# Kernel optimization log

Hardware: AMD Instinct MI355X
Metric: run time of the kernel (lower is better)

Reference implementation:

```python
import jax, jax.numpy as jnp
import numpy as np

RESO = 64
PAD = 0.1
SCALE = 8.0
PLANES = {'xz': (0, 2), 'xy': (0, 1), 'yz': (1, 2)}
PLANE_ORDER = ['xz', 'xy', 'yz']


def normalize_coordinate(p, plane):
    i, j = PLANES[plane]
    xy = jnp.stack([p[..., i], p[..., j]], axis=-1)
    xy = xy / (1.0 + PAD + 1e-3) + 0.5
    return jnp.clip(xy, 0.0, 1.0 - 1e-5)


def coordinate2index(xy, reso):
    x = (xy * reso).astype(jnp.int32)
    return x[..., 0] + reso * x[..., 1]  # (B, T)


def resblock(x, W0, b0, W1, b1, Ws):
    # ResnetBlockFC: fc_1(relu(fc_0(relu(x)))) + shortcut(x)
    net = jnp.maximum(x, 0.0) @ W0 + b0
    dx = jnp.maximum(net, 0.0) @ W1 + b1
    return x @ Ws + dx


def scatter_max_pool(c, idx_flat, num_seg):
    # c: (B, T, h); idx_flat: (B*T,) batch-offset plane indices
    B, T, h = c.shape
    pooled = jax.ops.segment_max(c.reshape(B * T, h), idx_flat, num_segments=num_seg)
    return pooled[idx_flat].reshape(B, T, h)


def plane_feature(p, c, plane):
    # scatter_mean of c into (B, c_dim, RESO, RESO); empty cells -> 0
    B, T, cd = c.shape
    R2 = RESO * RESO
    idx = coordinate2index(normalize_coordinate(p / SCALE, plane), RESO)
    idxf = (idx + jnp.arange(B, dtype=jnp.int32)[:, None] * R2).reshape(-1)
    sums = jax.ops.segment_sum(c.reshape(B * T, cd), idxf, num_segments=B * R2)
    cnt = jax.ops.segment_sum(jnp.ones((B * T,), c.dtype), idxf, num_segments=B * R2)
    mean = sums / jnp.maximum(cnt, 1.0)[:, None]
    return mean.reshape(B, R2, cd).transpose(0, 2, 1).reshape(B, cd, RESO, RESO)


def forward(p, fc_pos_W, fc_pos_b, blocks_W0, blocks_b0, blocks_W1, blocks_b1, blocks_Ws, fc_c_W, fc_c_b):
    B, T, _ = p.shape
    R2 = RESO * RESO
    offs = jnp.arange(B, dtype=jnp.int32)[:, None] * R2
    idx = {k: (coordinate2index(normalize_coordinate(p / SCALE, k), RESO) + offs).reshape(-1)
           for k in PLANE_ORDER}

    net = p @ fc_pos_W + fc_pos_b  # (B, T, 3h)
    net = resblock(net, blocks_W0[0], blocks_b0[0], blocks_W1[0], blocks_b1[0], blocks_Ws[0])
    n_blocks = blocks_W0.shape[0]
    for i in range(1, n_blocks):
        pooled = sum(scatter_max_pool(net, idx[k], B * R2) for k in PLANE_ORDER)
        meanp = jnp.broadcast_to(net.mean(axis=1, keepdims=True), net.shape)
        net = jnp.concatenate([net, pooled, meanp], axis=-1)  # (B, T, 3h)
        net = resblock(net, blocks_W0[i], blocks_b0[i], blocks_W1[i], blocks_b1[i], blocks_Ws[i])

    c = net @ fc_c_W + fc_c_b  # (B, T, c_dim)
    fea = jnp.stack([plane_feature(p, c, k) for k in PLANE_ORDER], axis=0)
    return fea  # (3, B, c_dim, RESO, RESO) in order xz, xy, yz


def setup_inputs() -> dict:
    key = jax.random.key(0)
    ks = jax.random.split(key, 10)
    B, T, dim = 16, 8192, 3
    h, c_dim, nb = 128, 128, 5
    s = 0.05
    return {
        'p': jax.random.normal(ks[0], (B, T, dim), jnp.float32) * 2.0,
        'fc_pos_W': jax.random.normal(ks[1], (dim, 3 * h), jnp.float32) * s,
        'fc_pos_b': jnp.zeros((3 * h,), jnp.float32),
        'blocks_W0': jax.random.normal(ks[2], (nb, 3 * h, h), jnp.float32) * s,
        'blocks_b0': jnp.zeros((nb, h), jnp.float32),
        'blocks_W1': jax.random.normal(ks[3], (nb, h, h), jnp.float32) * s,
        'blocks_b1': jnp.zeros((nb, h), jnp.float32),
        'blocks_Ws': jax.random.normal(ks[4], (nb, 3 * h, h), jnp.float32) * s,
        'fc_c_W': jax.random.normal(ks[5], (h, c_dim), jnp.float32) * s,
        'fc_c_b': jnp.zeros((c_dim,), jnp.float32),
    }


def reference(p, fc_pos_W, fc_pos_b, blocks_W0, blocks_b0, blocks_W1, blocks_b1, blocks_Ws, fc_c_W, fc_c_b):
    return forward(p, fc_pos_W, fc_pos_b, blocks_W0, blocks_b0, blocks_W1, blocks_b1, blocks_Ws, fc_c_W, fc_c_b)
```

## Files before the change

kernel.cpp:

```cpp
#include <hip/hip_runtime.h>

#define BT (16 * 8192)
#define NB 5
#define NCELL 65536
typedef unsigned int uint;
typedef unsigned short ushort;
typedef __attribute__((ext_vector_type(8))) _Float16 half8;
typedef __attribute__((ext_vector_type(2))) __fp16 fp16x2;
typedef __attribute__((ext_vector_type(2))) _Float16 half2v;
typedef __attribute__((ext_vector_type(4))) float f32x4;


__device__ __forceinline__ uint f2h2(float a, float b) {
    fp16x2 h = __builtin_amdgcn_cvt_pkrtz(a, b);
    return *(uint*)&h;
}
__device__ __forceinline__ float h2f_lo(uint u) { half2v h = *(half2v*)&u; return (float)h[0]; }
__device__ __forceinline__ float h2f_hi(uint u) { half2v h = *(half2v*)&u; return (float)h[1]; }
__device__ __forceinline__ uint pk_add(uint a, uint b) {
    uint d; asm("v_pk_add_f16 %0, %1, %2" : "=v"(d) : "v"(a), "v"(b)); return d;
}
__device__ __forceinline__ uint pk_max(uint a, uint b) {
    uint d; asm("v_pk_max_f16 %0, %1, %2" : "=v"(d) : "v"(a), "v"(b)); return d;
}

__device__ __forceinline__ uint relu2(uint u) {
    uint m = (u >> 15) & 0x00010001u;
    return u & ~(m * 0xffffu);
}
__device__ __forceinline__ half8 relu8(half8 a) {
    uint4 u = *(uint4*)&a;
    u.x = relu2(u.x); u.y = relu2(u.y); u.z = relu2(u.z); u.w = relu2(u.w);
    return *(half8*)&u;
}
__device__ __forceinline__ f32x4 bcast4(float x) { return (f32x4){x, x, x, x}; }
__device__ __forceinline__ f32x4 mfma16(half8 a, half8 b, f32x4 c) {
    return __builtin_amdgcn_mfma_f32_16x16x32_f16(a, b, c, 0, 0, 0);
}

__global__ void k_idx(const float* __restrict__ p, int* __restrict__ idx,
                      int4* __restrict__ idx4) {
    int r = blockIdx.x * 256 + threadIdx.x;
    if (r >= BT) return;
    float p0 = p[3 * r + 0], p1 = p[3 * r + 1], p2 = p[3 * r + 2];
    const float DEN = (float)(1.0 + 0.1 + 1e-3);
    const float HI  = (float)(1.0 - 1e-5);
    int b = r >> 13;
    float x0 = fminf(fmaxf((p0 / 8.0f) / DEN + 0.5f, 0.0f), HI);
    float x1 = fminf(fmaxf((p1 / 8.0f) / DEN + 0.5f, 0.0f), HI);
    float x2 = fminf(fmaxf((p2 / 8.0f) / DEN + 0.5f, 0.0f), HI);
    int i0 = (int)(x0 * 64.0f);
    int i1 = (int)(x1 * 64.0f);
    int i2 = (int)(x2 * 64.0f);
    int base = b << 12;
    int exz = base + i0 + (i2 << 6);
    int exy = base + i0 + (i1 << 6);
    int eyz = base + i1 + (i2 << 6);
    idx[r] = exz; idx[BT + r] = exy; idx[2 * BT + r] = eyz;
    idx4[r] = make_int4(exz, exy, eyz, 0);
}

__global__ void k_hist(const int* __restrict__ idx, int* __restrict__ cnt) {
    int r = blockIdx.x * 256 + threadIdx.x;
    if (r >= BT) return;
    atomicAdd(cnt + idx[r], 1);
    atomicAdd(cnt + NCELL + idx[BT + r], 1);
    atomicAdd(cnt + 2 * NCELL + idx[2 * BT + r], 1);
}

__global__ __launch_bounds__(1024) void k_scan(const int* __restrict__ cnt,
                                               int* __restrict__ starts,
                                               int* __restrict__ cursor) {
    __shared__ int sc[1024];
    int pl = blockIdx.x, t = threadIdx.x;
    const int* c = cnt + pl * NCELL;
    int base = t * 64;
    int s = 0;
    for (int i = 0; i < 64; ++i) s += c[base + i];
    sc[t] = s;
    __syncthreads();
    for (int off = 1; off < 1024; off <<= 1) {
        int v = (t >= off) ? sc[t - off] : 0;
        __syncthreads();
        sc[t] += v;
        __syncthreads();
    }
    int run = sc[t] - s;
    for (int i = 0; i < 64; ++i) {
        int cell = base + i;
        starts[pl * NCELL + cell] = run;
        cursor[pl * NCELL + cell] = run;
        run += c[cell];
    }
}

__global__ void k_scatter_order(const int* __restrict__ idx, int* __restrict__ cursor,
                                int* __restrict__ order, int* __restrict__ rank) {
    int r = blockIdx.x * 256 + threadIdx.x;
    if (r >= BT) return;
    for (int pl = 0; pl < 3; ++pl) {
        int cell = idx[pl * BT + r];
        int pos = atomicAdd(cursor + pl * NCELL + cell, 1);
        order[pl * BT + pos] = r;
        rank[pl * BT + r] = pos;
    }
}

__global__ void k_wconv(const float* __restrict__ W0, const float* __restrict__ W1,
                        const float* __restrict__ Ws, const float* __restrict__ Wc,
                        ushort* __restrict__ wb) {
    int mat = blockIdx.y;
    int K = (mat < 5 || (mat >= 10 && mat < 15)) ? 384 : 128;
    int e = blockIdx.x * 256 + threadIdx.x;
    if (e >= K * 128) return;
    const float* src;
    size_t doff;
    if (mat < 5)       { src = W0 + (size_t)mat * 49152;        doff = (size_t)mat * 49152; }
    else if (mat < 10) { src = W1 + (size_t)(mat - 5) * 16384;  doff = 245760 + (size_t)(mat - 5) * 16384; }
    else if (mat < 15) { src = Ws + (size_t)(mat - 10) * 49152; doff = 327680 + (size_t)(mat - 10) * 49152; }
    else               { src = Wc;                              doff = 573440; }
    int ko = e & 31, n = (e >> 5) & 127, kt = e >> 12;
    wb[doff + e] = (ushort)f2h2(src[(size_t)(kt * 32 + ko) * 128 + n], 0.0f);
}

__global__ __launch_bounds__(256) void k_segmax(const uint* __restrict__ netu,
                                                const int* __restrict__ starts,
                                                const int* __restrict__ cnt,
                                                const int* __restrict__ order,
                                                uint* __restrict__ segu,
                                                const float* __restrict__ meanPrev,
                                                const ushort* __restrict__ wb0,
                                                const float* __restrict__ b0v,
                                                const ushort* __restrict__ wbs,
                                                const float* __restrict__ b1v,
                                                float* __restrict__ rv0,
                                                float* __restrict__ rvS) {
    int t = threadIdx.x;
    if (blockIdx.x >= 12288) {
        __shared__ float ms[128];
        int b = blockIdx.x - 12288;
        if (t < 128) ms[t] = meanPrev[b * 128 + t];
        __syncthreads();
        if (t < 128) {
            float s0 = b0v[t], ss = b1v[t];
#pragma unroll 4
            for (int k = 0; k < 128; ++k) {
                float mv = ms[k];
                int kt = 8 + (k >> 5), ko = k & 31;
                float w0 = h2f_lo((uint)wb0[kt * 4096 + t * 32 + ko]);
                float ws = h2f_lo((uint)wbs[kt * 4096 + t * 32 + ko]);
                s0 = fmaf(fmaxf(mv, 0.0f), w0, s0);
                ss = fmaf(mv, ws, ss);
            }
            rv0[b * 128 + t] = s0;
            rvS[b * 128 + t] = ss;
        }
        return;
    }
    const int l = t & 63, wv = t >> 6;
    const int g0 = blockIdx.x * 16 + wv * 4;
    const int pl = g0 >> 16;
    const int* ordp = order + pl * BT;

    int n[4], st[4];
#pragma unroll
    for (int c = 0; c < 4; ++c) { n[c] = cnt[g0 + c]; st[c] = starts[g0 + c]; }

    uint v[4][4];
#pragma unroll
    for (int c = 0; c < 4; ++c) {
        if (n[c] > 0) {
            const int* op = ordp + st[c];
            int nm1 = n[c] - 1;
#pragma unroll
            for (int k = 0; k < 4; ++k) {
                int kk = k < nm1 ? k : nm1;
                v[c][k] = netu[(size_t)op[kk] * 64 + l];
            }
        }
    }
#pragma unroll
    for (int c = 0; c < 4; ++c) {
        if (n[c] > 0) {
            uint m = pk_max(pk_max(v[c][0], v[c][1]), pk_max(v[c][2], v[c][3]));
            const int* op = ordp + st[c];
            int nm1 = n[c] - 1;
            for (int k = 4; k < n[c]; k += 4) {
                int k1 = k + 1 < nm1 ? k + 1 : nm1;
                int k2 = k + 2 < nm1 ? k + 2 : nm1;
                int k3 = k + 3 < nm1 ? k + 3 : nm1;
                uint a = netu[(size_t)op[k] * 64 + l];
                uint b = netu[(size_t)op[k1] * 64 + l];
                uint cc = netu[(size_t)op[k2] * 64 + l];
                uint d = netu[(size_t)op[k3] * 64 + l];
                m = pk_max(m, pk_max(pk_max(a, b), pk_max(cc, d)));
            }
            segu[(size_t)(g0 + c) * 64 + l] = m;
        }
    }
}

template <int MODE>
__global__ __launch_bounds__(512, MODE == 0 ? 6 : 8) void k_resblock(
    const float* __restrict__ p, const uint* __restrict__ netu,
    const int4* __restrict__ idx4, const ushort* __restrict__ seg,
    const float* __restrict__ rv0, const float* __restrict__ rvS,
    const float* __restrict__ Wp, const float* __restrict__ bp,
    const ushort* __restrict__ wb0, const float* __restrict__ b0v,
    const ushort* __restrict__ wb1, const float* __restrict__ b1v,
    const ushort* __restrict__ wbs,
    ushort* __restrict__ out, float* __restrict__ meanW) {
    constexpr int LDA = (MODE == 0) ? 392 : 264;
    constexpr int NKT = (MODE == 0) ? 12 : 8;
    __shared__ __align__(16) ushort aT[64 * LDA];
    ushort* hT = aT;
    const int t = threadIdx.x;
    const int rowBase = blockIdx.x * 64;
    const int bb = rowBase >> 13;

    if constexpr (MODE == 0) {
        for (int f = t; f < 3072; f += 512) {
            int row = f / 48, g = f - row * 48;
            const float* pr = p + (size_t)(rowBase + row) * 3;
            float p0 = pr[0], p1 = pr[1], p2 = pr[2];
            int k0 = g * 8;
            uint d[4];
#pragma unroll
            for (int w = 0; w < 4; ++w) {
                int k = k0 + 2 * w;
                float v0 = bp[k]     + p0 * Wp[k]     + p1 * Wp[384 + k]     + p2 * Wp[768 + k];
                float v1 = bp[k + 1] + p0 * Wp[k + 1] + p1 * Wp[384 + k + 1] + p2 * Wp[768 + k + 1];
                d[w] = f2h2(v0, v1);
            }
            *(uint4*)(aT + row * LDA + k0) = make_uint4(d[0], d[1], d[2], d[3]);
        }
    } else {
        const uint4* nsrc = (const uint4*)netu;
#pragma unroll
        for (int i = 0; i < 2; ++i) {
            int f = t + 512 * i;
            int row = f >> 4, cu = f & 15;
            *(uint4*)(aT + row * LDA + cu * 8) = nsrc[(size_t)(rowBase + row) * 16 + cu];
        }
#pragma unroll
        for (int i = 0; i < 2; ++i) {
            int f = t + 512 * i;
            int row = f >> 4, grp = f & 15;
            int4 cc = idx4[rowBase + row];
            uint4 A = *(const uint4*)(seg + ((size_t)cc.x) * 128 + grp * 8);
            uint4 B = *(const uint4*)(seg + ((size_t)NCELL + cc.y) * 128 + grp * 8);
            uint4 C = *(const uint4*)(seg + ((size_t)2 * NCELL + cc.z) * 128 + grp * 8);
            uint4 d;
            d.x = pk_add(pk_add(A.x, B.x), C.x);
            d.y = pk_add(pk_add(A.y, B.y), C.y);
            d.z = pk_add(pk_add(A.z, B.z), C.z);
            d.w = pk_add(pk_add(A.w, B.w), C.w);
            *(uint4*)(aT + row * LDA + 128 + grp * 8) = d;
        }
    }
    __syncthreads();

    const int l = t & 63, wid = t >> 6;
    const int n0 = wid * 16;
    const int lm = l & 15, lg = l >> 4;
    const ushort* w0 = wb0 + n0 * 32;
    const ushort* w1 = wb1 + n0 * 32;
    const ushort* ws = wbs + n0 * 32;

    f32x4 acc0[4], accS[4];
    {
        float bi, si;
        if constexpr (MODE == 0) { bi = b0v[n0 + lm];            si = b1v[n0 + lm]; }
        else                     { bi = rv0[bb * 128 + n0 + lm]; si = rvS[bb * 128 + n0 + lm]; }
#pragma unroll
        for (int im = 0; im < 4; ++im) { acc0[im] = bcast4(bi); accS[im] = bcast4(si); }
    }
#pragma unroll
    for (int kt = 0; kt < NKT; ++kt) {
        half8 b0 = *(const half8*)(w0 + kt * 4096 + lm * 32 + lg * 8);
        half8 bs = *(const half8*)(ws + kt * 4096 + lm * 32 + lg * 8);
#pragma unroll
        for (int im = 0; im < 4; ++im) {
            half8 a = *(const half8*)(aT + (im * 16 + lm) * LDA + kt * 32 + lg * 8);
            acc0[im] = mfma16(relu8(a), b0, acc0[im]);
            accS[im] = mfma16(a, bs, accS[im]);
        }
    }
    __syncthreads();

#pragma unroll
    for (int im = 0; im < 4; ++im)
#pragma unroll
        for (int j = 0; j < 4; ++j) {
            int row = im * 16 + lg * 4 + j;
            hT[row * 136 + n0 + lm] = (ushort)f2h2(fmaxf(acc0[im][j], 0.0f), 0.0f);
        }
    __syncthreads();

#pragma unroll
    for (int kt = 0; kt < 4; ++kt) {
        half8 b = *(const half8*)(w1 + kt * 4096 + lm * 32 + lg * 8);
#pragma unroll
        for (int im = 0; im < 4; ++im) {
            half8 a = *(const half8*)(hT + (im * 16 + lm) * 136 + kt * 32 + lg * 8);
            accS[im] = mfma16(a, b, accS[im]);
        }
    }

#pragma unroll
    for (int im = 0; im < 4; ++im)
#pragma unroll
        for (int j = 0; j < 4; ++j) {
            int row = rowBase + im * 16 + lg * 4 + j;
            out[(size_t)row * 128 + n0 + lm] = (ushort)f2h2(accS[im][j], 0.0f);
        }

    if (meanW) {
        float s = 0.0f;
#pragma unroll
        for (int im = 0; im < 4; ++im)
#pragma unroll
            for (int j = 0; j < 4; ++j) s += accS[im][j];
        s += __shfl_xor(s, 16);
        s += __shfl_xor(s, 32);
        if (l < 16) atomicAdd(meanW + bb * 128 + n0 + l, s * (1.0f / 8192.0f));
    }
}

__device__ __forceinline__ void mfma_gemm3(const ushort* __restrict__ aLDS, int lda, int nk,
                                           const ushort* __restrict__ wb, int lm, int lg,
                                           f32x4 acc[4][2]) {
    for (int kt = 0; kt < nk; ++kt) {
        half8 b0 = *(const half8*)(wb + kt * 4096 + lm * 32 + lg * 8);
        half8 b1 = *(const half8*)(wb + kt * 4096 + (16 + lm) * 32 + lg * 8);
#pragma unroll
        for (int im = 0; im < 4; ++im) {
            half8 a = *(const half8*)(aLDS + (im * 16 + lm) * lda + kt * 32 + lg * 8);
            acc[im][0] = mfma16(a, b0, acc[im][0]);
            acc[im][1] = mfma16(a, b1, acc[im][1]);
        }
    }
}

__global__ __launch_bounds__(256, 2) void k_fcc(const uint* __restrict__ netu,
                                                const int* __restrict__ rank,
                                                const ushort* __restrict__ wbc,
                                                const float* __restrict__ bc,
                                                ushort* __restrict__ c3) {
    __shared__ __align__(16) ushort aT[64 * 136];
    __shared__ int rkS[3][64];
    const int t = threadIdx.x;
    const int rowBase = blockIdx.x * 64;
    if (t < 192) {
        int pl = t >> 6, rr = t & 63;
        rkS[pl][rr] = rank[pl * BT + rowBase + rr];
    }
    const uint4* nsrc = (const uint4*)netu;
#pragma unroll
    for (int i = 0; i < 4; ++i) {
        int u = t + 256 * i;
        int row = u >> 4, cu = u & 15;
        *(uint4*)(aT + row * 136 + cu * 8) = nsrc[(size_t)(rowBase + row) * 16 + cu];
    }
    __syncthreads();
    const int l = t & 63, wid = t >> 6;
    const int n0 = wid * 32;
    const int lm = l & 15, lg = l >> 4;
    f32x4 acc[4][2];
    {
        float ci0 = bc[n0 + lm], ci1 = bc[n0 + 16 + lm];
#pragma unroll
        for (int im = 0; im < 4; ++im) { acc[im][0] = bcast4(ci0); acc[im][1] = bcast4(ci1); }
    }
    mfma_gemm3(aT, 136, 4, wbc + n0 * 32, lm, lg, acc);
#pragma unroll
    for (int im = 0; im < 4; ++im)
#pragma unroll
        for (int ic = 0; ic < 2; ++ic)
#pragma unroll
            for (int j = 0; j < 4; ++j) {
                int row = im * 16 + lg * 4 + j;
                int col = n0 + ic * 16 + lm;
                ushort v = (ushort)f2h2(acc[im][ic][j], 0.0f);
                c3[(size_t)rkS[0][row] * 128 + col] = v;
                c3[((size_t)BT + rkS[1][row]) * 128 + col] = v;
                c3[((size_t)2 * BT + rkS[2][row]) * 128 + col] = v;
            }
}

__global__ __launch_bounds__(256) void k_segfin(const uint* __restrict__ c3,
                                                const int* __restrict__ starts,
                                                const int* __restrict__ cnt,
                                                float* __restrict__ out) {
    __shared__ float tile[64 * 130];
    const int t = threadIdx.x;
    const int w = t >> 6, l = t & 63;
    const int bx = blockIdx.x;
    const int pl = bx >> 10;
    const int rem = bx & 1023;
    const int b = rem >> 6;
    const int cl0 = (rem & 63) << 6;
    const int gbase = pl * NCELL + (b << 12) + cl0;

    for (int i = 0; i < 16; ++i) {
        int cellLocal = w * 16 + i;
        int g = gbase + cellLocal;
        int n = cnt[g];
        float s0 = 0.f, s1 = 0.f;
        if (n > 0) {
            size_t rowb = (size_t)pl * BT + starts[g];
            int j = 0;
            for (; j + 4 <= n; j += 4) {
                uint a = c3[(rowb + j) * 64 + l];
                uint bq = c3[(rowb + j + 1) * 64 + l];
                uint c = c3[(rowb + j + 2) * 64 + l];
                uint d = c3[(rowb + j + 3) * 64 + l];
                s0 += (h2f_lo(a) + h2f_lo(bq)) + (h2f_lo(c) + h2f_lo(d));
                s1 += (h2f_hi(a) + h2f_hi(bq)) + (h2f_hi(c) + h2f_hi(d));
            }
            int rm = n - j;
            if (rm > 0) {
                uint a = c3[(rowb + j) * 64 + l];
                uint bq = (rm > 1) ? c3[(rowb + j + 1) * 64 + l] : 0u;
                uint c = (rm > 2) ? c3[(rowb + j + 2) * 64 + l] : 0u;
                s0 += h2f_lo(a) + (h2f_lo(bq) + h2f_lo(c));
                s1 += h2f_hi(a) + (h2f_hi(bq) + h2f_hi(c));
            }
        }
        *(float2*)(tile + cellLocal * 130 + 2 * l) = make_float2(s0, s1);
    }
    __syncthreads();

    int cn = cnt[gbase + l];
    float inv = cn > 0 ? 1.0f / (float)cn : 0.0f;
    size_t obase = (((size_t)((pl * 16 + b) * 128)) << 12) + cl0 + l;
#pragma unroll 8
    for (int j = 0; j < 32; ++j) {
        int ch = w * 32 + j;
        out[obase + ((size_t)ch << 12)] = tile[l * 130 + ch] * inv;
    }
}

extern "C" void kernel_launch(void* const* d_in, const int* in_sizes, int n_in,
                              void* d_out, int out_size, void* d_ws, size_t ws_size,
                              hipStream_t stream) {
    const float* p  = (const float*)d_in[0];
    const float* Wp = (const float*)d_in[1];
    const float* bp = (const float*)d_in[2];
    const float* W0 = (const float*)d_in[3];
    const float* b0 = (const float*)d_in[4];
    const float* W1 = (const float*)d_in[5];
    const float* b1 = (const float*)d_in[6];
    const float* Ws = (const float*)d_in[7];
    const float* Wc = (const float*)d_in[8];
    const float* bc = (const float*)d_in[9];
    float* out = (float*)d_out;

    ushort* c3     = (ushort*)d_ws;
    ushort* seg    = c3;
    ushort* net    = c3 + 50331648;
    ushort* wb     = net + 16777216;
    int*    idx    = (int*)(wb + 589824);
    int*    order  = idx + 393216;
    int*    rank   = order + 393216;
    int*    cnt    = rank + 393216;
    int*    starts = cnt + 196608;
    int*    cursor = starts + 196608;
    int4*   idx4   = (int4*)(cursor + 196608);
    float*  meanB  = (float*)(idx4 + 131072);
    float*  rv0    = meanB + 4 * 2048;
    float*  rvS    = rv0 + 2048;

    k_idx<<<512, 256, 0, stream>>>(p, idx, idx4);
    (void)hipMemsetAsync(cnt, 0, 3 * NCELL * 4, stream);
    k_hist<<<512, 256, 0, stream>>>(idx, cnt);
    k_scan<<<3, 1024, 0, stream>>>(cnt, starts, cursor);
    k_scatter_order<<<512, 256, 0, stream>>>(idx, cursor, order, rank);
    k_wconv<<<dim3(192, 16), 256, 0, stream>>>(W0, W1, Ws, Wc, wb);
    (void)hipMemsetAsync(meanB, 0, 4 * 2048 * 4, stream);

    k_resblock<0><<<2048, 512, 0, stream>>>(
        p, nullptr, nullptr, nullptr, nullptr, nullptr, Wp, bp,
        wb, b0, wb + 245760, b1, wb + 327680, net, meanB);

    for (int i = 1; i < NB; ++i) {
        const ushort* wb0i = wb + (size_t)i * 49152;
        const ushort* wb1i = wb + 245760 + (size_t)i * 16384;
        const ushort* wbsi = wb + 327680 + (size_t)i * 49152;
        k_segmax<<<12304, 256, 0, stream>>>((const uint*)net, starts, cnt, order, (uint*)seg,
                                            meanB + (i - 1) * 2048, wb0i, b0 + i * 128,
                                            wbsi, b1 + i * 128, rv0, rvS);
        float* mw = (i < NB - 1) ? meanB + i * 2048 : nullptr;
        k_resblock<1><<<2048, 512, 0, stream>>>(
            nullptr, (const uint*)net, idx4, seg, rv0, rvS, nullptr, nullptr,
            wb0i, nullptr, wb1i, nullptr, wbsi, net, mw);
    }

    k_fcc<<<2048, 256, 0, stream>>>((const uint*)net, rank, wb + 573440, bc, c3);

    k_segfin<<<3072, 256, 0, stream>>>((const uint*)c3, starts, cnt, out);
}
```

Before: 658.0 us.

## Fold fc_pos into block-0 shortcut weights and use packed max for ReLU

In the first resblock the shortcut term (p@Wp+bp)@Ws0 is algebraically folded into a precomputed 3x128 matrix plus bias by a new tiny kernel, so MODE 0 skips 12 shortcut MFMA steps and their weight loads. It evaluates three FMAs per output instead. Point coordinates are staged in shared memory once per block, and the bit-mask ReLU is replaced with a packed fp16 max against zero. The folded shortcut is computed in fp32 from the unrounded inputs, so it differs slightly numerically from the fp16 path. It also adds a serial single-block launch.

Result: no change. 665.2 us (+1.1%).

```diff
diff --git a/kernel.cpp b/kernel.cpp
--- a/kernel.cpp
+++ b/kernel.cpp
@@ -24,13 +24,10 @@
     uint d; asm("v_pk_max_f16 %0, %1, %2" : "=v"(d) : "v"(a), "v"(b)); return d;
 }
 
-__device__ __forceinline__ uint relu2(uint u) {
-    uint m = (u >> 15) & 0x00010001u;
-    return u & ~(m * 0xffffu);
-}
 __device__ __forceinline__ half8 relu8(half8 a) {
     uint4 u = *(uint4*)&a;
-    u.x = relu2(u.x); u.y = relu2(u.y); u.z = relu2(u.z); u.w = relu2(u.w);
+    u.x = pk_max(u.x, 0u); u.y = pk_max(u.y, 0u);
+    u.z = pk_max(u.z, 0u); u.w = pk_max(u.w, 0u);
     return *(half8*)&u;
 }
 __device__ __forceinline__ f32x4 bcast4(float x) { return (f32x4){x, x, x, x}; }
@@ -121,6 +118,25 @@
     else               { src = Wc;                              doff = 573440; }
     int ko = e & 31, n = (e >> 5) & 127, kt = e >> 12;
     wb[doff + e] = (ushort)f2h2(src[(size_t)(kt * 32 + ko) * 128 + n], 0.0f);
+}
+
+__global__ __launch_bounds__(128) void k_pfold(const float* __restrict__ Wp,
+                                               const float* __restrict__ bp,
+                                               const float* __restrict__ Ws0,
+                                               const float* __restrict__ b1v,
+                                               float* __restrict__ M3,
+                                               float* __restrict__ bps) {
+    int n = threadIdx.x;
+    float s0 = 0.f, s1 = 0.f, s2 = 0.f, sb = b1v[n];
+    for (int k = 0; k < 384; ++k) {
+        float w = Ws0[(size_t)k * 128 + n];
+        s0 = fmaf(Wp[k], w, s0);
+        s1 = fmaf(Wp[384 + k], w, s1);
+        s2 = fmaf(Wp[768 + k], w, s2);
+        sb = fmaf(bp[k], w, sb);
+    }
+    M3[n] = s0; M3[128 + n] = s1; M3[256 + n] = s2;
+    bps[n] = sb;
 }
 
 __global__ __launch_bounds__(256) void k_segmax(const uint* __restrict__ netu,
@@ -206,6 +222,7 @@
     const int4* __restrict__ idx4, const ushort* __restrict__ seg,
     const float* __restrict__ rv0, const float* __restrict__ rvS,
     const float* __restrict__ Wp, const float* __restrict__ bp,
+    const float* __restrict__ M3, const float* __restrict__ bps,
     const ushort* __restrict__ wb0, const float* __restrict__ b0v,
     const ushort* __restrict__ wb1, const float* __restrict__ b1v,
     const ushort* __restrict__ wbs,
@@ -213,16 +230,18 @@
     constexpr int LDA = (MODE == 0) ? 392 : 264;
     constexpr int NKT = (MODE == 0) ? 12 : 8;
     __shared__ __align__(16) ushort aT[64 * LDA];
+    __shared__ float pS[MODE == 0 ? 192 : 1];
     ushort* hT = aT;
     const int t = threadIdx.x;
     const int rowBase = blockIdx.x * 64;
     const int bb = rowBase >> 13;
 
     if constexpr (MODE == 0) {
+        if (t < 192) pS[t] = p[(size_t)rowBase * 3 + t];
+        __syncthreads();
         for (int f = t; f < 3072; f += 512) {
             int row = f / 48, g = f - row * 48;
-            const float* pr = p + (size_t)(rowBase + row) * 3;
-            float p0 = pr[0], p1 = pr[1], p2 = pr[2];
+            float p0 = pS[row * 3 + 0], p1 = pS[row * 3 + 1], p2 = pS[row * 3 + 2];
             int k0 = g * 8;
             uint d[4];
 #pragma unroll
@@ -269,22 +288,41 @@
 
     f32x4 acc0[4], accS[4];
     {
-        float bi, si;
-        if constexpr (MODE == 0) { bi = b0v[n0 + lm];            si = b1v[n0 + lm]; }
-        else                     { bi = rv0[bb * 128 + n0 + lm]; si = rvS[bb * 128 + n0 + lm]; }
-#pragma unroll
-        for (int im = 0; im < 4; ++im) { acc0[im] = bcast4(bi); accS[im] = bcast4(si); }
+        float bi;
+        if constexpr (MODE == 0) bi = b0v[n0 + lm];
+        else                     bi = rv0[bb * 128 + n0 + lm];
+#pragma unroll
+        for (int im = 0; im < 4; ++im) acc0[im] = bcast4(bi);
+    }
+    if constexpr (MODE == 1) {
+        float si = rvS[bb * 128 + n0 + lm];
+#pragma unroll
+        for (int im = 0; im < 4; ++im) accS[im] = bcast4(si);
     }
 #pragma unroll
     for (int kt = 0; kt < NKT; ++kt) {
         half8 b0 = *(const half8*)(w0 + kt * 4096 + lm * 32 + lg * 8);
-        half8 bs = *(const half8*)(ws + kt * 4096 + lm * 32 + lg * 8);
+        half8 bs;
+        if constexpr (MODE == 1) bs = *(const half8*)(ws + kt * 4096 + lm * 32 + lg * 8);
 #pragma unroll
         for (int im = 0; im < 4; ++im) {
             half8 a = *(const half8*)(aT + (im * 16 + lm) * LDA + kt * 32 + lg * 8);
             acc0[im] = mfma16(relu8(a), b0, acc0[im]);
-            accS[im] = mfma16(a, bs, accS[im]);
-        }
+            if constexpr (MODE == 1) accS[im] = mfma16(a, bs, accS[im]);
+        }
+    }
+    if constexpr (MODE == 0) {
+        int col = n0 + lm;
+        float m0 = M3[col], m1 = M3[128 + col], m2 = M3[256 + col], bb2 = bps[col];
+#pragma unroll
+        for (int im = 0; im < 4; ++im)
+#pragma unroll
+            for (int j = 0; j < 4; ++j) {
+                int row = im * 16 + lg * 4 + j;
+                accS[im][j] = fmaf(pS[row * 3 + 0], m0,
+                              fmaf(pS[row * 3 + 1], m1,
+                              fmaf(pS[row * 3 + 2], m2, bb2)));
+            }
     }
     __syncthreads();
 
@@ -470,6 +508,8 @@
     float*  meanB  = (float*)(idx4 + 131072);
     float*  rv0    = meanB + 4 * 2048;
     float*  rvS    = rv0 + 2048;
+    float*  M3     = rvS + 2048;
+    float*  bps    = M3 + 384;
 
     k_idx<<<512, 256, 0, stream>>>(p, idx, idx4);
     (void)hipMemsetAsync(cnt, 0, 3 * NCELL * 4, stream);
@@ -477,10 +517,11 @@
     k_scan<<<3, 1024, 0, stream>>>(cnt, starts, cursor);
     k_scatter_order<<<512, 256, 0, stream>>>(idx, cursor, order, rank);
     k_wconv<<<dim3(192, 16), 256, 0, stream>>>(W0, W1, Ws, Wc, wb);
+    k_pfold<<<1, 128, 0, stream>>>(Wp, bp, Ws, b1, M3, bps);
     (void)hipMemsetAsync(meanB, 0, 4 * 2048 * 4, stream);
 
     k_resblock<0><<<2048, 512, 0, stream>>>(
-        p, nullptr, nullptr, nullptr, nullptr, nullptr, Wp, bp,
+        p, nullptr, nullptr, nullptr, nullptr, nullptr, Wp, bp, M3, bps,
         wb, b0, wb + 245760, b1, wb + 327680, net, meanB);
 
     for (int i = 1; i < NB; ++i) {
@@ -493,7 +534,7 @@
         float* mw = (i < NB - 1) ? meanB + i * 2048 : nullptr;
         k_resblock<1><<<2048, 512, 0, stream>>>(
             nullptr, (const uint*)net, idx4, seg, rv0, rvS, nullptr, nullptr,
-            wb0i, nullptr, wb1i, nullptr, wbsi, net, mw);
+            nullptr, nullptr, wb0i, nullptr, wb1i, nullptr, wbsi, net, mw);
     }
 
     k_fcc<<<2048, 256, 0, stream>>>((const uint*)net, rank, wb + 573440, bc, c3);
```
